# Performance work log

Measured on AMD Instinct MI355X. Metric: run time of the kernel, lower is better.

The kernel has to match this reference:

```python
import jax, jax.numpy as jnp
import numpy as np
from jax import lax

T = 4          # num_steps
TAU = 2.0      # spikingjelly LIFNode default tau
VTH = 1.0      # v_threshold
ALPHA = 2.0    # ATan surrogate default alpha
EPS = 1e-5     # BatchNorm eps

@jax.custom_vjp
def atan_spike(x):
    # Heaviside forward, ATan surrogate backward (spikingjelly surrogate.ATan)
    return (x >= 0.0).astype(x.dtype)

def _atan_fwd(x):
    return atan_spike(x), x

def _atan_bwd(x, g):
    sg = (ALPHA / 2.0) / (1.0 + (jnp.pi / 2.0 * ALPHA * x) ** 2)
    return (g * sg,)

atan_spike.defvjp(_atan_fwd, _atan_bwd)

def lif_multistep(x_seq):
    # x_seq: (T, B, D, L). LIF with decay_input=True, v_reset=0.0, hard reset,
    # detach_reset=True (reset spike is stop-gradiented).
    def step(v, xt):
        h = v + (xt - v) / TAU          # membrane charge
        s = atan_spike(h - VTH)          # spike
        v_new = h * (1.0 - lax.stop_gradient(s))  # hard reset to 0
        return v_new, s
    _, spikes = lax.scan(step, jnp.zeros_like(x_seq[0]), x_seq)
    return spikes  # (T, B, D, L)

def setup_inputs() -> dict:
    key = jax.random.key(0)
    k1, k2, k3, k4 = jax.random.split(key, 4)
    L, TB, D = 2048, 128, 128
    x = jax.random.normal(k1, (L, TB, D), dtype=jnp.float32)
    conv_w = jax.random.normal(k2, (D, D, 3), dtype=jnp.float32) * 0.05
    bn_gamma = jnp.ones((D,), jnp.float32)
    bn_beta = jnp.zeros((D,), jnp.float32)
    bn_mean = jax.random.normal(k3, (D,), dtype=jnp.float32) * 0.1
    bn_var = jax.random.uniform(k4, (D,), dtype=jnp.float32, minval=0.5, maxval=1.5)
    return {"x": x, "conv_w": conv_w, "bn_gamma": bn_gamma, "bn_beta": bn_beta,
            "bn_mean": bn_mean, "bn_var": bn_var}

def reference(x, conv_w, bn_gamma, bn_beta, bn_mean, bn_var):
    # x: (L, TB, D)
    L, TB, D = x.shape
    xf = jnp.transpose(x, (1, 2, 0))  # (TB, D, L)
    # Conv1d(D, D, k=3, stride=1, pad=1, bias=False)
    xf = lax.conv_general_dilated(xf, conv_w, window_strides=(1,),
                                  padding=((1, 1),),
                                  dimension_numbers=("NCH", "OIH", "NCH"))
    # BatchNorm1d in inference mode (running stats)
    scale = bn_gamma * lax.rsqrt(bn_var + EPS)
    xf = (xf - bn_mean[None, :, None]) * scale[None, :, None] + bn_beta[None, :, None]
    # (TB, D, L) -> (T, B, D, L), multi-step LIF
    xs = xf.reshape(T, TB // T, D, L)
    sp = lif_multistep(xs)
    sp = sp.reshape(TB, D, L)   # flatten(0, 1); dropout is identity in eval
    return x + jnp.transpose(sp, (2, 0, 1))  # (L, TB, D)
```

## Files before the change

kernel.cpp:

```cpp
#include <hip/hip_runtime.h>


constexpr int L   = 2048;
constexpr int NTB = 128;
constexpr int D   = 128;
constexpr int T   = 4;
constexpr int LT  = 64;
constexpr int NP  = LT + 2;
constexpr int JT  = 8;

__global__ __launch_bounds__(256, 3)
void snn_conv_lif(const float* __restrict__ x, const float* __restrict__ w,
                  const float* __restrict__ gamma, const float* __restrict__ beta,
                  const float* __restrict__ mean, const float* __restrict__ var,
                  float* __restrict__ out) {
    __shared__ float xs[NP * 64];
    __shared__ float ws[2][768 * 4];

    const int tid = threadIdx.x;
    const int b   = blockIdx.x & 31;
    const int lt  = blockIdx.x >> 5;
    const int l0  = lt * LT;
    const int q4  = tid & 31;
    const int p0  = (tid >> 6) * 16 + ((tid >> 5) & 1) * JT;
    const float4* x4 = (const float4*)x;

    int wgoff[3], wloff[3];
    #pragma unroll
    for (int r = 0; r < 3; ++r) {
        const int idx = tid + r * 256;
        const int qq  = idx & 31;
        const int cc  = idx >> 5;
        const int f   = cc >> 2;
        const int oo  = cc & 3;
        wgoff[r] = (4 * qq + oo) * (D * 3) + f * 4;
        wloff[r] = ((oo * 6 + f) * 32 + qq) * 4;
    }

    float sc[4], bi[4];
    {
        const float4 g4 = ((const float4*)gamma)[q4];
        const float4 b4 = ((const float4*)beta)[q4];
        const float4 m4 = ((const float4*)mean)[q4];
        const float4 v4 = ((const float4*)var)[q4];
        const float gg[4] = {g4.x, g4.y, g4.z, g4.w};
        const float bb[4] = {b4.x, b4.y, b4.z, b4.w};
        const float mm[4] = {m4.x, m4.y, m4.z, m4.w};
        const float vv[4] = {v4.x, v4.y, v4.z, v4.w};
        #pragma unroll
        for (int oo = 0; oo < 4; ++oo) {
            sc[oo] = gg[oo] / sqrtf(vv[oo] + 1e-5f);
            bi[oo] = bb[oo] - mm[oo] * sc[oo];
        }
    }

    float v[4][JT];
    #pragma unroll
    for (int oo = 0; oo < 4; ++oo)
        #pragma unroll
        for (int j = 0; j < JT; ++j) v[oo][j] = 0.f;

    #pragma unroll
    for (int r = 0; r < 3; ++r)
        *((float4*)(&ws[0][wloff[r]])) = *((const float4*)(w + wgoff[r]));

    #pragma unroll 1
    for (int t = 0; t < T; ++t) {
        const int n = t * 32 + b;

        float a[4][JT];
        #pragma unroll
        for (int oo = 0; oo < 4; ++oo)
            #pragma unroll
            for (int j = 0; j < JT; ++j) a[oo][j] = 0.f;

        #pragma unroll 1
        for (int half = 0; half < 2; ++half) {
            const int cb = half * 16;
            for (int idx = tid; idx < NP * 16; idx += 256) {
                const int p = idx >> 4, c = idx & 15;
                const int ll = l0 - 1 + p;
                float4 val = make_float4(0.f, 0.f, 0.f, 0.f);
                if (ll >= 0 && ll < L)
                    val = x4[(ll * NTB + n) * 32 + cb + c];
                ((float4*)xs)[p * 16 + c] = val;
            }
            __syncthreads();

            #pragma unroll 1
            for (int itl = 0; itl < 8; ++itl) {
                const int it  = half * 8 + itl;
                const int itn = (it + 1) & 15;
                float4 wp[3];
                #pragma unroll
                for (int r = 0; r < 3; ++r)
                    wp[r] = *((const float4*)(w + wgoff[r] + itn * 24));

                const float* wsb = ws[it & 1];
                #pragma unroll
                for (int i4 = 0; i4 < 2; ++i4) {
                    float4 W0[4], W1[4], W2[4];
                    #pragma unroll
                    for (int oo = 0; oo < 4; ++oo) {
                        const float* wpt = wsb + ((oo * 6 + i4 * 3) * 32 + q4) * 4;
                        W0[oo] = *((const float4*)(wpt));
                        W1[oo] = *((const float4*)(wpt + 128));
                        W2[oo] = *((const float4*)(wpt + 256));
                    }

                    const int iic = itl * 2 + i4;
                    const float4* xcol = (const float4*)xs + iic;
                    float4 xa = xcol[(p0 + 0) * 16];
                    float4 xb = xcol[(p0 + 1) * 16];
                    #pragma unroll
                    for (int j = 0; j < JT; ++j) {
                        const float4 xc = xcol[(p0 + j + 2) * 16];
                        #pragma unroll
                        for (int oo = 0; oo < 4; ++oo) {
                            float s = a[oo][j];
                            const float4 w0 = W0[oo], w1 = W1[oo], w2 = W2[oo];
                            s = fmaf(xa.x, w0.x, s);
                            s = fmaf(xa.y, w0.w, s);
                            s = fmaf(xa.z, w1.z, s);
                            s = fmaf(xa.w, w2.y, s);
                            s = fmaf(xb.x, w0.y, s);
                            s = fmaf(xb.y, w1.x, s);
                            s = fmaf(xb.z, w1.w, s);
                            s = fmaf(xb.w, w2.z, s);
                            s = fmaf(xc.x, w0.z, s);
                            s = fmaf(xc.y, w1.y, s);
                            s = fmaf(xc.z, w2.x, s);
                            s = fmaf(xc.w, w2.w, s);
                            a[oo][j] = s;
                        }
                        xa = xb; xb = xc;
                    }
                }

                float* wsn = ws[itn & 1];
                #pragma unroll
                for (int r = 0; r < 3; ++r)
                    *((float4*)(&wsn[wloff[r]])) = wp[r];
                __syncthreads();
            }
        }

        #pragma unroll
        for (int j = 0; j < JT; ++j) {
            const int l = l0 + p0 + j;
            const float4 res = x4[(l * NTB + n) * 32 + q4];
            const float rr[4] = {res.x, res.y, res.z, res.w};
            float ov[4];
            #pragma unroll
            for (int oo = 0; oo < 4; ++oo) {
                const float y = fmaf(a[oo][j], sc[oo], bi[oo]);
                const float h = 0.5f * (v[oo][j] + y);
                const bool fire = (h >= 1.0f);
                v[oo][j] = fire ? 0.0f : h;
                ov[oo] = rr[oo] + (fire ? 1.0f : 0.0f);
            }
            ((float4*)out)[(l * NTB + n) * 32 + q4] =
                make_float4(ov[0], ov[1], ov[2], ov[3]);
        }
    }
}

extern "C" void kernel_launch(void* const* d_in, const int* in_sizes, int n_in,
                              void* d_out, int out_size, void* d_ws, size_t ws_size,
                              hipStream_t stream) {
    const float* x     = (const float*)d_in[0];
    const float* w     = (const float*)d_in[1];
    const float* gamma = (const float*)d_in[2];
    const float* beta  = (const float*)d_in[3];
    const float* mean  = (const float*)d_in[4];
    const float* var   = (const float*)d_in[5];
    float* out = (float*)d_out;

    dim3 grid((L / LT) * 32);
    dim3 block(256);
    snn_conv_lif<<<grid, block, 0, stream>>>(x, w, gamma, beta, mean, var, out);
}
```

Measured before the change: 543.3 us.

## Process two time steps per pass to reuse conv weights across samples

The conv now computes two timesteps (batch entries n and n+32) together. Each weight fragment loaded from shared memory feeds twice as many FMAs, and the weight streaming and syncs per channel chunk are halved. The cost is double the accumulator registers and a doubled x tile in shared memory, so launch bounds drop from 3 to 2 blocks per CU, which reduces occupancy.

```diff
diff --git a/kernel.cpp b/kernel.cpp
--- a/kernel.cpp
+++ b/kernel.cpp
@@ -9,12 +9,12 @@
 constexpr int NP  = LT + 2;
 constexpr int JT  = 8;
 
-__global__ __launch_bounds__(256, 3)
+__global__ __launch_bounds__(256, 2)
 void snn_conv_lif(const float* __restrict__ x, const float* __restrict__ w,
                   const float* __restrict__ gamma, const float* __restrict__ beta,
                   const float* __restrict__ mean, const float* __restrict__ var,
                   float* __restrict__ out) {
-    __shared__ float xs[NP * 64];
+    __shared__ float xs[2][NP * 16 * 4];
     __shared__ float ws[2][768 * 4];
 
     const int tid = threadIdx.x;
@@ -64,87 +64,8 @@
     for (int r = 0; r < 3; ++r)
         *((float4*)(&ws[0][wloff[r]])) = *((const float4*)(w + wgoff[r]));
 
-    #pragma unroll 1
-    for (int t = 0; t < T; ++t) {
+    auto epi = [&](const float (&a)[4][JT], int t) {
         const int n = t * 32 + b;
-
-        float a[4][JT];
-        #pragma unroll
-        for (int oo = 0; oo < 4; ++oo)
-            #pragma unroll
-            for (int j = 0; j < JT; ++j) a[oo][j] = 0.f;
-
-        #pragma unroll 1
-        for (int half = 0; half < 2; ++half) {
-            const int cb = half * 16;
-            for (int idx = tid; idx < NP * 16; idx += 256) {
-                const int p = idx >> 4, c = idx & 15;
-                const int ll = l0 - 1 + p;
-                float4 val = make_float4(0.f, 0.f, 0.f, 0.f);
-                if (ll >= 0 && ll < L)
-                    val = x4[(ll * NTB + n) * 32 + cb + c];
-                ((float4*)xs)[p * 16 + c] = val;
-            }
-            __syncthreads();
-
-            #pragma unroll 1
-            for (int itl = 0; itl < 8; ++itl) {
-                const int it  = half * 8 + itl;
-                const int itn = (it + 1) & 15;
-                float4 wp[3];
-                #pragma unroll
-                for (int r = 0; r < 3; ++r)
-                    wp[r] = *((const float4*)(w + wgoff[r] + itn * 24));
-
-                const float* wsb = ws[it & 1];
-                #pragma unroll
-                for (int i4 = 0; i4 < 2; ++i4) {
-                    float4 W0[4], W1[4], W2[4];
-                    #pragma unroll
-                    for (int oo = 0; oo < 4; ++oo) {
-                        const float* wpt = wsb + ((oo * 6 + i4 * 3) * 32 + q4) * 4;
-                        W0[oo] = *((const float4*)(wpt));
-                        W1[oo] = *((const float4*)(wpt + 128));
-                        W2[oo] = *((const float4*)(wpt + 256));
-                    }
-
-                    const int iic = itl * 2 + i4;
-                    const float4* xcol = (const float4*)xs + iic;
-                    float4 xa = xcol[(p0 + 0) * 16];
-                    float4 xb = xcol[(p0 + 1) * 16];
-                    #pragma unroll
-                    for (int j = 0; j < JT; ++j) {
-                        const float4 xc = xcol[(p0 + j + 2) * 16];
-                        #pragma unroll
-                        for (int oo = 0; oo < 4; ++oo) {
-                            float s = a[oo][j];
-                            const float4 w0 = W0[oo], w1 = W1[oo], w2 = W2[oo];
-                            s = fmaf(xa.x, w0.x, s);
-                            s = fmaf(xa.y, w0.w, s);
-                            s = fmaf(xa.z, w1.z, s);
-                            s = fmaf(xa.w, w2.y, s);
-                            s = fmaf(xb.x, w0.y, s);
-                            s = fmaf(xb.y, w1.x, s);
-                            s = fmaf(xb.z, w1.w, s);
-                            s = fmaf(xb.w, w2.z, s);
-                            s = fmaf(xc.x, w0.z, s);
-                            s = fmaf(xc.y, w1.y, s);
-                            s = fmaf(xc.z, w2.x, s);
-                            s = fmaf(xc.w, w2.w, s);
-                            a[oo][j] = s;
-                        }
-                        xa = xb; xb = xc;
-                    }
-                }
-
-                float* wsn = ws[itn & 1];
-                #pragma unroll
-                for (int r = 0; r < 3; ++r)
-                    *((float4*)(&wsn[wloff[r]])) = wp[r];
-                __syncthreads();
-            }
-        }
-
         #pragma unroll
         for (int j = 0; j < JT; ++j) {
             const int l = l0 + p0 + j;
@@ -162,6 +83,119 @@
             ((float4*)out)[(l * NTB + n) * 32 + q4] =
                 make_float4(ov[0], ov[1], ov[2], ov[3]);
         }
+    };
+
+    #pragma unroll 1
+    for (int tp = 0; tp < 2; ++tp) {
+        const int n0 = (tp * 2) * 32 + b;
+        const int n1 = n0 + 32;
+
+        float a0[4][JT], a1[4][JT];
+        #pragma unroll
+        for (int oo = 0; oo < 4; ++oo)
+            #pragma unroll
+            for (int j = 0; j < JT; ++j) { a0[oo][j] = 0.f; a1[oo][j] = 0.f; }
+
+        #pragma unroll 1
+        for (int half = 0; half < 2; ++half) {
+            const int cb = half * 16;
+            for (int idx = tid; idx < NP * 16; idx += 256) {
+                const int p = idx >> 4, c = idx & 15;
+                const int ll = l0 - 1 + p;
+                float4 v0 = make_float4(0.f, 0.f, 0.f, 0.f);
+                float4 v1 = make_float4(0.f, 0.f, 0.f, 0.f);
+                if (ll >= 0 && ll < L) {
+                    v0 = x4[(ll * NTB + n0) * 32 + cb + c];
+                    v1 = x4[(ll * NTB + n1) * 32 + cb + c];
+                }
+                ((float4*)(&xs[0][0]))[p * 16 + c] = v0;
+                ((float4*)(&xs[1][0]))[p * 16 + c] = v1;
+            }
+            __syncthreads();
+
+            #pragma unroll 1
+            for (int itl = 0; itl < 8; ++itl) {
+                const int it  = half * 8 + itl;
+                const int itn = (it + 1) & 15;
+                float4 wp[3];
+                #pragma unroll
+                for (int r = 0; r < 3; ++r)
+                    wp[r] = *((const float4*)(w + wgoff[r] + itn * 24));
+
+                const float* wsb = ws[it & 1];
+                #pragma unroll
+                for (int i4 = 0; i4 < 2; ++i4) {
+                    float4 W0[4], W1[4], W2[4];
+                    #pragma unroll
+                    for (int oo = 0; oo < 4; ++oo) {
+                        const float* wpt = wsb + ((oo * 6 + i4 * 3) * 32 + q4) * 4;
+                        W0[oo] = *((const float4*)(wpt));
+                        W1[oo] = *((const float4*)(wpt + 128));
+                        W2[oo] = *((const float4*)(wpt + 256));
+                    }
+
+                    const int iic = itl * 2 + i4;
+                    const float4* xcol0 = (const float4*)(&xs[0][0]) + iic;
+                    const float4* xcol1 = (const float4*)(&xs[1][0]) + iic;
+                    float4 xa0 = xcol0[(p0 + 0) * 16];
+                    float4 xb0 = xcol0[(p0 + 1) * 16];
+                    float4 xa1 = xcol1[(p0 + 0) * 16];
+                    float4 xb1 = xcol1[(p0 + 1) * 16];
+                    #pragma unroll
+                    for (int j = 0; j < JT; ++j) {
+                        const float4 xc0 = xcol0[(p0 + j + 2) * 16];
+                        const float4 xc1 = xcol1[(p0 + j + 2) * 16];
+                        #pragma unroll
+                        for (int oo = 0; oo < 4; ++oo) {
+                            float s = a0[oo][j];
+                            const float4 w0 = W0[oo], w1 = W1[oo], w2 = W2[oo];
+                            s = fmaf(xa0.x, w0.x, s);
+                            s = fmaf(xa0.y, w0.w, s);
+                            s = fmaf(xa0.z, w1.z, s);
+                            s = fmaf(xa0.w, w2.y, s);
+                            s = fmaf(xb0.x, w0.y, s);
+                            s = fmaf(xb0.y, w1.x, s);
+                            s = fmaf(xb0.z, w1.w, s);
+                            s = fmaf(xb0.w, w2.z, s);
+                            s = fmaf(xc0.x, w0.z, s);
+                            s = fmaf(xc0.y, w1.y, s);
+                            s = fmaf(xc0.z, w2.x, s);
+                            s = fmaf(xc0.w, w2.w, s);
+                            a0[oo][j] = s;
+                        }
+                        #pragma unroll
+                        for (int oo = 0; oo < 4; ++oo) {
+                            float s = a1[oo][j];
+                            const float4 w0 = W0[oo], w1 = W1[oo], w2 = W2[oo];
+                            s = fmaf(xa1.x, w0.x, s);
+                            s = fmaf(xa1.y, w0.w, s);
+                            s = fmaf(xa1.z, w1.z, s);
+                            s = fmaf(xa1.w, w2.y, s);
+                            s = fmaf(xb1.x, w0.y, s);
+                            s = fmaf(xb1.y, w1.x, s);
+                            s = fmaf(xb1.z, w1.w, s);
+                            s = fmaf(xb1.w, w2.z, s);
+                            s = fmaf(xc1.x, w0.z, s);
+                            s = fmaf(xc1.y, w1.y, s);
+                            s = fmaf(xc1.z, w2.x, s);
+                            s = fmaf(xc1.w, w2.w, s);
+                            a1[oo][j] = s;
+                        }
+                        xa0 = xb0; xb0 = xc0;
+                        xa1 = xb1; xb1 = xc1;
+                    }
+                }
+
+                float* wsn = ws[itn & 1];
+                #pragma unroll
+                for (int r = 0; r < 3; ++r)
+                    *((float4*)(&wsn[wloff[r]])) = wp[r];
+                __syncthreads();
+            }
+        }
+
+        epi(a0, tp * 2);
+        epi(a1, tp * 2 + 1);
     }
 }
 
```

After: 672.0 us. +23.7%, slower.
